# Kernel optimization log

Measured on AMD Instinct MI355X. Metric: run time of the kernel, lower is better.

The kernel has to match this reference:

```python
import jax, jax.numpy as jnp
import numpy as np

HID, NH, NKV, HD = 2048, 16, 8, 128
EPS = 1e-6
THETA = 10000.0
SCALE = HD ** -0.5


def setup_inputs() -> dict:
    key = jax.random.key(0)
    ks = jax.random.split(key, 6)
    S = 2048
    return {
        "positions": jnp.arange(S, dtype=jnp.int32),
        "hidden_states": jax.random.normal(ks[0], (S, HID), dtype=jnp.float32),
        "layernorm_weight": jax.random.uniform(ks[1], (HID,), dtype=jnp.float32, minval=0.5, maxval=1.5),
        "w_qkv": jax.random.normal(ks[2], ((NH + 2 * NKV) * HD, HID), dtype=jnp.float32) * 0.02,
        "w_o": jax.random.normal(ks[3], (HID, NH * HD), dtype=jnp.float32) * 0.02,
        "q_norm_w": jax.random.uniform(ks[4], (HD,), dtype=jnp.float32, minval=0.5, maxval=1.5),
        "k_norm_w": jax.random.uniform(ks[5], (HD,), dtype=jnp.float32, minval=0.5, maxval=1.5),
    }


def _rmsnorm(x, w, eps=EPS):
    var = jnp.mean(jnp.square(x), axis=-1, keepdims=True)
    return x * jax.lax.rsqrt(var + eps) * w


def _rope(x, cos, sin):
    # x: [S, h, HD]; cos/sin: [S, 1, HD//2] (neox-style rotate-half)
    x1, x2 = x[..., : HD // 2], x[..., HD // 2 :]
    return jnp.concatenate([x1 * cos - x2 * sin, x2 * cos + x1 * sin], axis=-1)


def reference(positions, hidden_states, layernorm_weight, w_qkv, w_o, q_norm_w, k_norm_w):
    S = hidden_states.shape[0]
    # Fused RMSNorm + QKV projection
    hn = _rmsnorm(hidden_states, layernorm_weight)
    qkv = hn @ w_qkv.T  # [S, (NH+2*NKV)*HD]
    q, k, v = jnp.split(qkv, [NH * HD, (NH + NKV) * HD], axis=-1)
    q = q.reshape(S, NH, HD)
    k = k.reshape(S, NKV, HD)
    v = v.reshape(S, NKV, HD)
    # Per-head QK RMSNorm
    q = _rmsnorm(q, q_norm_w)
    k = _rmsnorm(k, k_norm_w)
    # RoPE
    inv_freq = 1.0 / (THETA ** (jnp.arange(0, HD, 2, dtype=jnp.float32) / HD))
    freqs = positions.astype(jnp.float32)[:, None] * inv_freq  # [S, HD//2]
    cos = jnp.cos(freqs)[:, None, :]
    sin = jnp.sin(freqs)[:, None, :]
    q = _rope(q, cos, sin)
    k = _rope(k, cos, sin)
    # GQA: expand kv heads to match query heads
    rep = NH // NKV
    k = jnp.repeat(k, rep, axis=1)  # [S, NH, HD]
    v = jnp.repeat(v, rep, axis=1)
    # Causal attention
    scores = jnp.einsum("shd,thd->hst", q, k) * SCALE  # [NH, S, S]
    causal = jnp.tril(jnp.ones((S, S), dtype=bool))
    scores = jnp.where(causal, scores, jnp.finfo(scores.dtype).min)
    probs = jax.nn.softmax(scores, axis=-1)
    out = jnp.einsum("hst,thd->shd", probs, v)  # [S, NH, HD]
    # Output projection
    return out.reshape(S, NH * HD) @ w_o.T
```

## Files before the change

kernel.cpp:

```cpp
#include <hip/hip_runtime.h>
#include <hip/hip_bf16.h>
#include <math.h>

#define HID 2048
#define NH 16
#define NKV 8
#define HD 128
#define SEQ 2048
#define EPS 1e-6f
#define THETA 10000.0f
#define SCALE 0.08838834764831845f

typedef __attribute__((ext_vector_type(8))) short bf8_t;
typedef __attribute__((ext_vector_type(4))) float f4_t;

__device__ __forceinline__ short f2bf(float f) {
    union { __hip_bfloat16 h; short s; } u;
    u.h = __float2bfloat16(f);
    return u.s;
}
__device__ __forceinline__ float bf2f(short s) {
    union { short s; __hip_bfloat16 h; } u;
    u.s = s;
    return __bfloat162float(u.h);
}
__device__ __forceinline__ bf8_t pack8(const float4& a, const float4& b) {
    bf8_t r;
    r[0] = f2bf(a.x); r[1] = f2bf(a.y); r[2] = f2bf(a.z); r[3] = f2bf(a.w);
    r[4] = f2bf(b.x); r[5] = f2bf(b.y); r[6] = f2bf(b.z); r[7] = f2bf(b.w);
    return r;
}
__device__ __forceinline__ void gload16(const short* g, short* l) {
    __builtin_amdgcn_global_load_lds(
        (const __attribute__((address_space(1))) unsigned int*)g,
        (__attribute__((address_space(3))) unsigned int*)l, 16, 0, 0);
}

__device__ __forceinline__ float wave_reduce_sum(float v) {
#pragma unroll
    for (int off = 32; off > 0; off >>= 1) v += __shfl_xor(v, off);
    return v;
}

__global__ __launch_bounds__(256) void prep_kernel(
    const float* __restrict__ w_qkv, short* __restrict__ wqb,
    const float* __restrict__ w_o, short* __restrict__ wob,
    const float* __restrict__ x, const float* __restrict__ w,
    short* __restrict__ out) {
    int bid = blockIdx.x;
    int tid = threadIdx.x;
    if (bid < 4096) {
        int i = bid * 256 + tid;
        float4 a = *(const float4*)(w_qkv + (size_t)i * 8);
        float4 b = *(const float4*)(w_qkv + (size_t)i * 8 + 4);
        *(bf8_t*)(wqb + (size_t)i * 8) = pack8(a, b);
        return;
    }
    if (bid < 6144) {
        int i = (bid - 4096) * 256 + tid;
        float4 a = *(const float4*)(w_o + (size_t)i * 8);
        float4 b = *(const float4*)(w_o + (size_t)i * 8 + 4);
        *(bf8_t*)(wob + (size_t)i * 8) = pack8(a, b);
        return;
    }
    int row = bid - 6144;
    const float* xr = x + (size_t)row * HID;
    float4 a = *(const float4*)(xr + tid * 8);
    float4 b = *(const float4*)(xr + tid * 8 + 4);
    float ss = a.x * a.x + a.y * a.y + a.z * a.z + a.w * a.w +
               b.x * b.x + b.y * b.y + b.z * b.z + b.w * b.w;
    ss = wave_reduce_sum(ss);
    __shared__ float part[4];
    __shared__ float s_scale;
    if ((tid & 63) == 0) part[tid >> 6] = ss;
    __syncthreads();
    if (tid == 0) {
        float t = part[0] + part[1] + part[2] + part[3];
        s_scale = rsqrtf(t / (float)HID + EPS);
    }
    __syncthreads();
    float sc = s_scale;
    float4 wa = *(const float4*)(w + tid * 8);
    float4 wb = *(const float4*)(w + tid * 8 + 4);
    float4 oa = make_float4(a.x * sc * wa.x, a.y * sc * wa.y,
                            a.z * sc * wa.z, a.w * sc * wa.w);
    float4 ob = make_float4(b.x * sc * wb.x, b.y * sc * wb.y,
                            b.z * sc * wb.z, b.w * sc * wb.w);
    *(bf8_t*)(out + (size_t)row * HID + tid * 8) = pack8(oa, ob);
}

template <int MODE>
__global__ __launch_bounds__(256) void gemm_mfma_kernel(
    const short* __restrict__ A, const short* __restrict__ B,
    float* __restrict__ C0, float* __restrict__ C1,
    short* __restrict__ Q, short* __restrict__ Kp,
    short* __restrict__ Vr, int M, int N, int K) {
    __shared__ short As[128][64];
    __shared__ short Bs[128][64];
    int tid = threadIdx.x;
    int wv = tid >> 6, lane = tid & 63;
    int n16 = lane & 15, qd = lane >> 4;
    int m0 = blockIdx.y * 128, n0 = blockIdx.x * 128;
    int wm = (wv >> 1) * 64, wn = (wv & 1) * 64;
    int sr8 = lane >> 3, slot = lane & 7;

    int kbeg, kend;
    float* Cf;
    if (MODE == 0) {
        int z = blockIdx.z;
        kbeg = z ? (K >> 1) : 0;
        kend = z ? K : (K >> 1);
        Cf = z ? C1 : C0;
    } else {
        kbeg = 0; kend = K; Cf = nullptr;
    }

    size_t ainv[4], binv[4];
#pragma unroll
    for (int it = 0; it < 4; ++it) {
        int row = wv * 32 + it * 8 + sr8;
        int chunk = (slot - row) & 7;
        ainv[it] = (size_t)(m0 + row) * K + chunk * 8;
        binv[it] = (size_t)(n0 + row) * K + chunk * 8;
    }

    f4_t acc[4][4];
#pragma unroll
    for (int i = 0; i < 4; ++i)
#pragma unroll
        for (int j = 0; j < 4; ++j) acc[i][j] = (f4_t){0.f, 0.f, 0.f, 0.f};

    for (int k0 = kbeg; k0 < kend; k0 += 64) {
        __syncthreads();
#pragma unroll
        for (int it = 0; it < 4; ++it) {
            gload16(A + ainv[it] + k0, &As[wv * 32 + it * 8][0]);
            gload16(B + binv[it] + k0, &Bs[wv * 32 + it * 8][0]);
        }
        __syncthreads();

        bf8_t af[4][2], bf[4][2];
#pragma unroll
        for (int t = 0; t < 4; ++t)
#pragma unroll
            for (int ks = 0; ks < 2; ++ks) {
                int ar = wm + t * 16 + n16;
                af[t][ks] = *(const bf8_t*)&As[ar][(((ks * 4 + qd) + ar) & 7) * 8];
                int br = wn + t * 16 + n16;
                bf[t][ks] = *(const bf8_t*)&Bs[br][(((ks * 4 + qd) + br) & 7) * 8];
            }
#pragma unroll
        for (int ks = 0; ks < 2; ++ks)
#pragma unroll
            for (int mt = 0; mt < 4; ++mt)
#pragma unroll
                for (int nt = 0; nt < 4; ++nt)
                    acc[mt][nt] = __builtin_amdgcn_mfma_f32_16x16x32_bf16(
                        af[mt][ks], bf[nt][ks], acc[mt][nt], 0, 0, 0);
    }

#pragma unroll
    for (int mt = 0; mt < 4; ++mt)
#pragma unroll
        for (int nt = 0; nt < 4; ++nt)
#pragma unroll
            for (int r = 0; r < 4; ++r) {
                int gm = m0 + wm + mt * 16 + qd * 4 + r;
                int gn = n0 + wn + nt * 16 + n16;
                float v = acc[mt][nt][r];
                if (MODE == 0) {
                    Cf[(size_t)gm * N + gn] = v;
                } else {
                    if (gn < NH * HD)
                        Q[(size_t)gm * (NH * HD) + gn] = f2bf(v);
                    else if (gn < (NH + NKV) * HD)
                        Kp[(size_t)gm * (NKV * HD) + (gn - NH * HD)] = f2bf(v);
                    else
                        Vr[(size_t)gm * (NKV * HD) + (gn - (NH + NKV) * HD)] = f2bf(v);
                }
            }
}

__global__ __launch_bounds__(256) void splitk_reduce_kernel(
    const float* __restrict__ p0, const float* __restrict__ p1,
    float* __restrict__ o) {
    size_t i = ((size_t)blockIdx.x * 256 + threadIdx.x) * 8;
    float4 a0 = *(const float4*)(p0 + i);
    float4 a1 = *(const float4*)(p0 + i + 4);
    float4 b0 = *(const float4*)(p1 + i);
    float4 b1 = *(const float4*)(p1 + i + 4);
    *(float4*)(o + i) =
        make_float4(a0.x + b0.x, a0.y + b0.y, a0.z + b0.z, a0.w + b0.w);
    *(float4*)(o + i + 4) =
        make_float4(a1.x + b1.x, a1.y + b1.y, a1.z + b1.z, a1.w + b1.w);
}

__global__ __launch_bounds__(256) void mid_kernel(
    const short* __restrict__ vr, short* __restrict__ vt,
    short* __restrict__ q, short* __restrict__ k,
    const float* __restrict__ qw, const float* __restrict__ kw,
    const int* __restrict__ pos) {
    int bid = blockIdx.x;
    int tid = threadIdx.x;
    if (bid < 512) {
        __shared__ short t[64][64];
        int s0 = (bid & 31) * 64, d0 = (bid >> 5) * 64;
        int sl = tid >> 3, ch = tid & 7;
#pragma unroll
        for (int it = 0; it < 2; ++it) {
            int s_local = it * 32 + sl;
            bf8_t vv = *(const bf8_t*)(vr + (size_t)(s0 + s_local) * (NKV * HD) + d0 + ch * 8);
            *(bf8_t*)&t[s_local][((ch + s_local) & 7) * 8] = vv;
        }
        __syncthreads();
#pragma unroll
        for (int it = 0; it < 2; ++it) {
            int d_local = it * 32 + sl;
            int sbase = ch * 8;
            bf8_t o;
#pragma unroll
            for (int j = 0; j < 8; ++j) {
                int s = sbase + j;
                o[j] = t[s][(((d_local >> 3) + s) & 7) * 8 + (d_local & 7)];
            }
            *(bf8_t*)(vt + (size_t)(d0 + d_local) * SEQ + s0 + sbase) = o;
        }
        return;
    }
    int u = (bid - 512) * 2 + (tid >> 7);
    int ui = tid >> 7, d = tid & 127;
    int s = u / 24, hh = u % 24;
    short* ptr;
    const float* w;
    if (hh < NH) {
        ptr = q + (size_t)s * (NH * HD) + hh * HD;
        w = qw;
    } else {
        ptr = k + (size_t)s * (NKV * HD) + (hh - NH) * HD;
        w = kw;
    }
    float x = bf2f(ptr[d]);
    float ss = wave_reduce_sum(x * x);
    __shared__ float part[2][2];
    if ((d & 63) == 0) part[ui][d >> 6] = ss;
    __syncthreads();
    float tot = part[ui][0] + part[ui][1];
    float xn = x * rsqrtf(tot / (float)HD + EPS) * w[d];
    __shared__ float sh[2][HD];
    sh[ui][d] = xn;
    __syncthreads();
    int j = d & 63;
    float inv = __expf((float)j * -0.14391156831f);
    float fr = (float)pos[s] * inv;
    float sn, cs;
    __sincosf(fr, &sn, &cs);
    float o;
    if (d < 64)
        o = xn * cs - sh[ui][d + 64] * sn;
    else
        o = xn * cs + sh[ui][d - 64] * sn;
    ptr[d] = f2bf(o);
}

__device__ __forceinline__ void attn_stage(
    short (&kb)[64][128], short (&vb)[128][64],
    const short* __restrict__ kg, const short* __restrict__ vg,
    int t0, const int (&kinv)[4], const int (&vinv)[4], int wv) {
#pragma unroll
    for (int it = 0; it < 4; ++it) {
        gload16(kg + (size_t)t0 * (NKV * HD) + kinv[it], &kb[wv * 16 + it * 4][0]);
        gload16(vg + t0 + vinv[it], &vb[wv * 32 + it * 8][0]);
    }
}

__device__ __forceinline__ void attn_tile(
    const short (&kb)[64][128], const short (&vb)[128][64],
    short (&psh)[4][2][16][64],
    const bf8_t (&qf)[2][4], f4_t (&of)[2][8],
    float (&m_i)[2][4], float (&l_p)[2][4],
    int wv, int n, int qd, int koff) {
    f4_t sc[2][4];
#pragma unroll
    for (int g = 0; g < 2; ++g)
#pragma unroll
        for (int kk = 0; kk < 4; ++kk) sc[g][kk] = (f4_t){0.f, 0.f, 0.f, 0.f};
#pragma unroll
    for (int kk = 0; kk < 4; ++kk) {
        int key = kk * 16 + n;
#pragma unroll
        for (int ks = 0; ks < 4; ++ks) {
            bf8_t kf = *(const bf8_t*)&kb[key][(((ks * 4 + qd) + key) & 15) * 8];
            sc[0][kk] = __builtin_amdgcn_mfma_f32_16x16x32_bf16(qf[0][ks], kf, sc[0][kk], 0, 0, 0);
            sc[1][kk] = __builtin_amdgcn_mfma_f32_16x16x32_bf16(qf[1][ks], kf, sc[1][kk], 0, 0, 0);
        }
    }
#pragma unroll
    for (int g = 0; g < 2; ++g) {
        int rows0 = wv * 32 + g * 16;
        bool needm = (koff + 63 > rows0);
#pragma unroll
        for (int kk = 0; kk < 4; ++kk)
#pragma unroll
            for (int r = 0; r < 4; ++r) {
                float s = sc[g][kk][r] * SCALE;
                if (needm && (koff + kk * 16 + n > rows0 + qd * 4 + r)) s = -1e30f;
                sc[g][kk][r] = s;
            }
#pragma unroll
        for (int r = 0; r < 4; ++r) {
            float mx = fmaxf(fmaxf(sc[g][0][r], sc[g][1][r]),
                             fmaxf(sc[g][2][r], sc[g][3][r]));
#pragma unroll
            for (int off = 1; off < 16; off <<= 1) mx = fmaxf(mx, __shfl_xor(mx, off));
            float mnew = fmaxf(m_i[g][r], mx);
            float al = __expf(m_i[g][r] - mnew);
            m_i[g][r] = mnew;
            float lsum = 0.f;
            int row = qd * 4 + r;
#pragma unroll
            for (int kk = 0; kk < 4; ++kk) {
                float p = __expf(sc[g][kk][r] - mnew);
                psh[wv][g][row][((kk * 16 + n) + row * 8) & 63] = f2bf(p);
                lsum += p;
            }
            l_p[g][r] = l_p[g][r] * al + lsum;
#pragma unroll
            for (int nb = 0; nb < 8; ++nb) of[g][nb][r] *= al;
        }
    }
    __builtin_amdgcn_wave_barrier();
#pragma unroll
    for (int ks2 = 0; ks2 < 2; ++ks2) {
        bf8_t pf0 = *(const bf8_t*)&psh[wv][0][n][((ks2 * 32 + qd * 8) + n * 8) & 63];
        bf8_t pf1 = *(const bf8_t*)&psh[wv][1][n][((ks2 * 32 + qd * 8) + n * 8) & 63];
#pragma unroll
        for (int nb = 0; nb < 8; ++nb) {
            int dim = nb * 16 + n;
            bf8_t vf = *(const bf8_t*)&vb[dim][(((ks2 * 4 + qd) + dim) & 7) * 8];
            of[0][nb] = __builtin_amdgcn_mfma_f32_16x16x32_bf16(pf0, vf, of[0][nb], 0, 0, 0);
            of[1][nb] = __builtin_amdgcn_mfma_f32_16x16x32_bf16(pf1, vf, of[1][nb], 0, 0, 0);
        }
    }
}

__global__ __launch_bounds__(256, 2) void attn_chunk_kernel(
    const short* __restrict__ q, const short* __restrict__ k,
    const short* __restrict__ vt, short* __restrict__ opart,
    float* __restrict__ ml) {
    __shared__ short kbufA[64][128], kbufB[64][128];
    __shared__ short vbufA[128][64], vbufB[128][64];
    __shared__ short psh[4][2][16][64];

    int tid = threadIdx.x;
    int wv = tid >> 6, lane = tid & 63;
    int n = lane & 15, qd = lane >> 4;

    int i = blockIdx.x;
    int hs = i >> 8, p = i & 255;
    int h = p >> 4;
    int qt = hs ? (p & 15) : (15 - (p & 15));
    int c = hs;
    int qbase = qt * 128;
    int tstart = c ? (qt + 1) : 0;
    int tcount = qt + 1;
    int kvh = h >> 1;

    int kinv[4], vinv[4];
#pragma unroll
    for (int it = 0; it < 4; ++it) {
        int key = wv * 16 + it * 4 + (lane >> 4);
        int ck = ((lane & 15) - key) & 15;
        kinv[it] = key * (NKV * HD) + kvh * HD + ck * 8;
        int dim = wv * 32 + it * 8 + (lane >> 3);
        int cv = ((lane & 7) - dim) & 7;
        vinv[it] = (kvh * HD + dim) * SEQ + cv * 8;
    }

    bf8_t qf[2][4];
#pragma unroll
    for (int g = 0; g < 2; ++g) {
        const short* qp =
            q + (size_t)(qbase + wv * 32 + g * 16 + n) * (NH * HD) + h * HD + qd * 8;
#pragma unroll
        for (int ks = 0; ks < 4; ++ks) qf[g][ks] = *(const bf8_t*)(qp + ks * 32);
    }

    f4_t of[2][8];
#pragma unroll
    for (int g = 0; g < 2; ++g)
#pragma unroll
        for (int x = 0; x < 8; ++x) of[g][x] = (f4_t){0.f, 0.f, 0.f, 0.f};
    float m_i[2][4] = {{-1e30f, -1e30f, -1e30f, -1e30f},
                       {-1e30f, -1e30f, -1e30f, -1e30f}};
    float l_p[2][4] = {{0.f, 0.f, 0.f, 0.f}, {0.f, 0.f, 0.f, 0.f}};

    attn_stage(kbufA, vbufA, k, vt, tstart * 64, kinv, vinv, wv);
    for (int tt = 0; tt < tcount; tt += 2) {
        __syncthreads();
        if (tt + 1 < tcount)
            attn_stage(kbufB, vbufB, k, vt, (tstart + tt + 1) * 64, kinv, vinv, wv);
        attn_tile(kbufA, vbufA, psh, qf, of, m_i, l_p, wv, n, qd,
                  (tstart + tt) * 64 - qbase);
        if (tt + 1 < tcount) {
            __syncthreads();
            if (tt + 2 < tcount)
                attn_stage(kbufA, vbufA, k, vt, (tstart + tt + 2) * 64, kinv, vinv, wv);
            attn_tile(kbufB, vbufB, psh, qf, of, m_i, l_p, wv, n, qd,
                      (tstart + tt + 1) * 64 - qbase);
        }
    }

    float lred[2][4];
#pragma unroll
    for (int g = 0; g < 2; ++g)
#pragma unroll
        for (int r = 0; r < 4; ++r) {
            float l = l_p[g][r];
#pragma unroll
            for (int off = 1; off < 16; off <<= 1) l += __shfl_xor(l, off);
            lred[g][r] = l;
        }

    size_t pb = ((size_t)(h * 16 + qt)) * 2 + c;
    short* op = opart + pb * (128 * 128);
#pragma unroll
    for (int g = 0; g < 2; ++g)
#pragma unroll
        for (int nb = 0; nb < 8; ++nb)
#pragma unroll
            for (int r = 0; r < 4; ++r) {
                int rl = wv * 32 + g * 16 + qd * 4 + r;
                op[rl * 128 + nb * 16 + n] = f2bf(of[g][nb][r]);
            }
    if (n == 0) {
#pragma unroll
        for (int g = 0; g < 2; ++g)
#pragma unroll
            for (int r = 0; r < 4; ++r) {
                int rl = wv * 32 + g * 16 + qd * 4 + r;
                ml[pb * 256 + rl * 2] = m_i[g][r];
                ml[pb * 256 + rl * 2 + 1] = lred[g][r];
            }
    }
}

__global__ __launch_bounds__(256) void attn_merge_kernel(
    const short* __restrict__ opart, const float* __restrict__ ml,
    short* __restrict__ o) {
    int bid = blockIdx.x;
    int h = bid >> 4, qt = bid & 15;
    int tid = threadIdx.x;
    int r = tid >> 1, hf = tid & 1;
    size_t pb0 = ((size_t)(h * 16 + qt)) * 2;
    size_t pb1 = pb0 + 1;
    float m0 = ml[pb0 * 256 + r * 2], l0 = ml[pb0 * 256 + r * 2 + 1];
    float m1 = ml[pb1 * 256 + r * 2], l1 = ml[pb1 * 256 + r * 2 + 1];
    float M = fmaxf(m0, m1);
    float w0 = __expf(m0 - M), w1 = __expf(m1 - M);
    float invL = 1.0f / (w0 * l0 + w1 * l1);
    int row = qt * 128 + r;
#pragma unroll
    for (int j = 0; j < 8; ++j) {
        int d0 = hf * 64 + j * 8;
        bf8_t a = *(const bf8_t*)(opart + pb0 * (128 * 128) + r * 128 + d0);
        bf8_t b = *(const bf8_t*)(opart + pb1 * (128 * 128) + r * 128 + d0);
        bf8_t e;
#pragma unroll
        for (int x = 0; x < 8; ++x)
            e[x] = f2bf((w0 * bf2f(a[x]) + w1 * bf2f(b[x])) * invL);
        *(bf8_t*)(o + (size_t)row * (NH * HD) + h * HD + d0) = e;
    }
}

extern "C" void kernel_launch(void* const* d_in, const int* in_sizes, int n_in,
                              void* d_out, int out_size, void* d_ws, size_t ws_size,
                              hipStream_t stream) {
    const int* positions   = (const int*)d_in[0];
    const float* hidden    = (const float*)d_in[1];
    const float* ln_w      = (const float*)d_in[2];
    const float* w_qkv     = (const float*)d_in[3];
    const float* w_o       = (const float*)d_in[4];
    const float* q_norm_w  = (const float*)d_in[5];
    const float* k_norm_w  = (const float*)d_in[6];
    float* out = (float*)d_out;

    char* base = (char*)d_ws;
    short* hnb   = (short*)(base);
    short* wqb   = (short*)(base + ((size_t)8 << 20));
    short* vtb   = (short*)(base + ((size_t)8 << 20));
    float* mlbuf = (float*)(base + ((size_t)12 << 20));
    short* wob   = (short*)(base + ((size_t)24 << 20));
    short* qbf   = (short*)(base + ((size_t)32 << 20));
    short* kbf   = (short*)(base + ((size_t)40 << 20));
    short* vrow  = (short*)(base + ((size_t)44 << 20));
    short* opart = (short*)d_out;
    float* p0 = (float*)(base + ((size_t)8 << 20));
    float* p1 = (float*)(base + ((size_t)32 << 20));

    prep_kernel<<<8192, 256, 0, stream>>>(w_qkv, wqb, w_o, wob, hidden, ln_w, hnb);
    gemm_mfma_kernel<1><<<dim3(32, 16), 256, 0, stream>>>(
        hnb, wqb, nullptr, nullptr, qbf, kbf, vrow, SEQ, (NH + 2 * NKV) * HD, HID);
    mid_kernel<<<512 + 24576, 256, 0, stream>>>(
        vrow, vtb, qbf, kbf, q_norm_w, k_norm_w, positions);
    attn_chunk_kernel<<<512, 256, 0, stream>>>(qbf, kbf, vtb, opart, mlbuf);
    attn_merge_kernel<<<256, 256, 0, stream>>>(opart, mlbuf, hnb);
    gemm_mfma_kernel<0><<<dim3(16, 16, 2), 256, 0, stream>>>(
        hnb, wob, p0, p1, nullptr, nullptr, nullptr, SEQ, NH * HD, HID);
    splitk_reduce_kernel<<<2048, 256, 0, stream>>>(p0, p1, out);
}
```

Measured before the change: 273.1 us.

## Transpose QK^T MFMA layout, add lazy softmax rescale and MFMA priority hints

Swaps the MFMA operands for the score product so each lane holds a single query row. This lets the row max and sum use two cross-lane shuffles instead of four, and keeps one running max/sum per lane instead of four. The softmax scale is folded into the exponent. The output rescale is skipped when the new max stays within a threshold of the old one (a lazy-rescale trick), and probabilities are packed four at a time into shared memory. s_setprio hints are added around the MFMA loops, and the merge now receives the max pre-scaled.

```diff
diff --git a/kernel.cpp b/kernel.cpp
--- a/kernel.cpp
+++ b/kernel.cpp
@@ -10,8 +10,10 @@
 #define EPS 1e-6f
 #define THETA 10000.0f
 #define SCALE 0.08838834764831845f
+#define DTHR 90.50966799187809f
 
 typedef __attribute__((ext_vector_type(8))) short bf8_t;
+typedef __attribute__((ext_vector_type(4))) short bf4_t;
 typedef __attribute__((ext_vector_type(4))) float f4_t;
 
 __device__ __forceinline__ short f2bf(float f) {
@@ -277,58 +279,72 @@
     const short (&kb)[64][128], const short (&vb)[128][64],
     short (&psh)[4][2][16][64],
     const bf8_t (&qf)[2][4], f4_t (&of)[2][8],
-    float (&m_i)[2][4], float (&l_p)[2][4],
+    float (&m_i)[2], float (&l_p)[2],
     int wv, int n, int qd, int koff) {
     f4_t sc[2][4];
 #pragma unroll
     for (int g = 0; g < 2; ++g)
 #pragma unroll
         for (int kk = 0; kk < 4; ++kk) sc[g][kk] = (f4_t){0.f, 0.f, 0.f, 0.f};
+    __builtin_amdgcn_s_setprio(1);
 #pragma unroll
     for (int kk = 0; kk < 4; ++kk) {
         int key = kk * 16 + n;
 #pragma unroll
         for (int ks = 0; ks < 4; ++ks) {
             bf8_t kf = *(const bf8_t*)&kb[key][(((ks * 4 + qd) + key) & 15) * 8];
-            sc[0][kk] = __builtin_amdgcn_mfma_f32_16x16x32_bf16(qf[0][ks], kf, sc[0][kk], 0, 0, 0);
-            sc[1][kk] = __builtin_amdgcn_mfma_f32_16x16x32_bf16(qf[1][ks], kf, sc[1][kk], 0, 0, 0);
-        }
-    }
+            sc[0][kk] = __builtin_amdgcn_mfma_f32_16x16x32_bf16(kf, qf[0][ks], sc[0][kk], 0, 0, 0);
+            sc[1][kk] = __builtin_amdgcn_mfma_f32_16x16x32_bf16(kf, qf[1][ks], sc[1][kk], 0, 0, 0);
+        }
+    }
+    __builtin_amdgcn_s_setprio(0);
 #pragma unroll
     for (int g = 0; g < 2; ++g) {
         int rows0 = wv * 32 + g * 16;
-        bool needm = (koff + 63 > rows0);
-#pragma unroll
-        for (int kk = 0; kk < 4; ++kk)
+        int qrow = rows0 + n;
+        if (koff + 63 > rows0) {
+#pragma unroll
+            for (int kk = 0; kk < 4; ++kk)
+#pragma unroll
+                for (int r = 0; r < 4; ++r)
+                    if (koff + kk * 16 + qd * 4 + r > qrow) sc[g][kk][r] = -1e30f;
+        }
+        float m01 = fmaxf(fmaxf(fmaxf(sc[g][0][0], sc[g][0][1]), fmaxf(sc[g][0][2], sc[g][0][3])),
+                          fmaxf(fmaxf(sc[g][1][0], sc[g][1][1]), fmaxf(sc[g][1][2], sc[g][1][3])));
+        float m23 = fmaxf(fmaxf(fmaxf(sc[g][2][0], sc[g][2][1]), fmaxf(sc[g][2][2], sc[g][2][3])),
+                          fmaxf(fmaxf(sc[g][3][0], sc[g][3][1]), fmaxf(sc[g][3][2], sc[g][3][3])));
+        float mx = fmaxf(m01, m23);
+        mx = fmaxf(mx, __shfl_xor(mx, 16));
+        mx = fmaxf(mx, __shfl_xor(mx, 32));
+        if (!__all(mx <= m_i[g] + DTHR)) {
+            float mnew = fmaxf(m_i[g], mx);
+            float al = __expf((m_i[g] - mnew) * SCALE);
+            m_i[g] = mnew;
+            l_p[g] *= al;
 #pragma unroll
             for (int r = 0; r < 4; ++r) {
-                float s = sc[g][kk][r] * SCALE;
-                if (needm && (koff + kk * 16 + n > rows0 + qd * 4 + r)) s = -1e30f;
-                sc[g][kk][r] = s;
+                float alr = __shfl(al, qd * 4 + r);
+#pragma unroll
+                for (int nb = 0; nb < 8; ++nb) of[g][nb][r] *= alr;
             }
-#pragma unroll
-        for (int r = 0; r < 4; ++r) {
-            float mx = fmaxf(fmaxf(sc[g][0][r], sc[g][1][r]),
-                             fmaxf(sc[g][2][r], sc[g][3][r]));
-#pragma unroll
-            for (int off = 1; off < 16; off <<= 1) mx = fmaxf(mx, __shfl_xor(mx, off));
-            float mnew = fmaxf(m_i[g][r], mx);
-            float al = __expf(m_i[g][r] - mnew);
-            m_i[g][r] = mnew;
-            float lsum = 0.f;
-            int row = qd * 4 + r;
-#pragma unroll
-            for (int kk = 0; kk < 4; ++kk) {
-                float p = __expf(sc[g][kk][r] - mnew);
-                psh[wv][g][row][((kk * 16 + n) + row * 8) & 63] = f2bf(p);
+        }
+        float mcur = m_i[g];
+        float lsum = 0.f;
+#pragma unroll
+        for (int kk = 0; kk < 4; ++kk) {
+            bf4_t pk;
+#pragma unroll
+            for (int r = 0; r < 4; ++r) {
+                float p = __expf((sc[g][kk][r] - mcur) * SCALE);
                 lsum += p;
+                pk[r] = f2bf(p);
             }
-            l_p[g][r] = l_p[g][r] * al + lsum;
-#pragma unroll
-            for (int nb = 0; nb < 8; ++nb) of[g][nb][r] *= al;
-        }
+            *(bf4_t*)&psh[wv][g][n][(kk * 16 + qd * 4 + n * 8) & 63] = pk;
+        }
+        l_p[g] += lsum;
     }
     __builtin_amdgcn_wave_barrier();
+    __builtin_amdgcn_s_setprio(1);
 #pragma unroll
     for (int ks2 = 0; ks2 < 2; ++ks2) {
         bf8_t pf0 = *(const bf8_t*)&psh[wv][0][n][((ks2 * 32 + qd * 8) + n * 8) & 63];
@@ -341,6 +357,7 @@
             of[1][nb] = __builtin_amdgcn_mfma_f32_16x16x32_bf16(pf1, vf, of[1][nb], 0, 0, 0);
         }
     }
+    __builtin_amdgcn_s_setprio(0);
 }
 
 __global__ __launch_bounds__(256, 2) void attn_chunk_kernel(
@@ -390,9 +407,8 @@
     for (int g = 0; g < 2; ++g)
 #pragma unroll
         for (int x = 0; x < 8; ++x) of[g][x] = (f4_t){0.f, 0.f, 0.f, 0.f};
-    float m_i[2][4] = {{-1e30f, -1e30f, -1e30f, -1e30f},
-                       {-1e30f, -1e30f, -1e30f, -1e30f}};
-    float l_p[2][4] = {{0.f, 0.f, 0.f, 0.f}, {0.f, 0.f, 0.f, 0.f}};
+    float m_i[2] = {-1e30f, -1e30f};
+    float l_p[2] = {0.f, 0.f};
 
     attn_stage(kbufA, vbufA, k, vt, tstart * 64, kinv, vinv, wv);
     for (int tt = 0; tt < tcount; tt += 2) {
@@ -410,16 +426,14 @@
         }
     }
 
-    float lred[2][4];
-#pragma unroll
-    for (int g = 0; g < 2; ++g)
-#pragma unroll
-        for (int r = 0; r < 4; ++r) {
-            float l = l_p[g][r];
-#pragma unroll
-            for (int off = 1; off < 16; off <<= 1) l += __shfl_xor(l, off);
-            lred[g][r] = l;
-        }
+    float lred[2];
+#pragma unroll
+    for (int g = 0; g < 2; ++g) {
+        float l = l_p[g];
+        l += __shfl_xor(l, 16);
+        l += __shfl_xor(l, 32);
+        lred[g] = l;
+    }
 
     size_t pb = ((size_t)(h * 16 + qt)) * 2 + c;
     short* op = opart + pb * (128 * 128);
@@ -432,15 +446,13 @@
                 int rl = wv * 32 + g * 16 + qd * 4 + r;
                 op[rl * 128 + nb * 16 + n] = f2bf(of[g][nb][r]);
             }
-    if (n == 0) {
-#pragma unroll
-        for (int g = 0; g < 2; ++g)
-#pragma unroll
-            for (int r = 0; r < 4; ++r) {
-                int rl = wv * 32 + g * 16 + qd * 4 + r;
-                ml[pb * 256 + rl * 2] = m_i[g][r];
-                ml[pb * 256 + rl * 2 + 1] = lred[g][r];
-            }
+    if (qd == 0) {
+#pragma unroll
+        for (int g = 0; g < 2; ++g) {
+            int rl = wv * 32 + g * 16 + n;
+            ml[pb * 256 + rl * 2] = m_i[g] * SCALE;
+            ml[pb * 256 + rl * 2 + 1] = lred[g];
+        }
     }
 }
 
```

After: 259.4 us. 5.0% less time.
